# Kernel tuning notes

Measured on AMD Instinct MI355X. Metric: run time of the kernel, lower is better.

The kernel has to match this reference:

```python
import jax, jax.numpy as jnp
import numpy as np

GROUPS = 4
SF = 2   # scale_factor
K = 3    # filter_k

def conv1x1(x, w, b):
    return jnp.einsum('bchw,oc->bohw', x, w) + b[None, :, None, None]

def grid_sample(img, grid):
    # img: (N,C,H,W); grid: (N,Hg,Wg,2) xy in [-1,1]; bilinear, border padding, align_corners=False
    N, C, H, W = img.shape
    ix = jnp.clip(((grid[..., 0] + 1.0) * W - 1.0) * 0.5, 0.0, W - 1.0)
    iy = jnp.clip(((grid[..., 1] + 1.0) * H - 1.0) * 0.5, 0.0, H - 1.0)
    x0 = jnp.floor(ix); y0 = jnp.floor(iy)
    wx = (ix - x0)[..., None]; wy = (iy - y0)[..., None]
    x0i = x0.astype(jnp.int32); y0i = y0.astype(jnp.int32)
    x1i = jnp.minimum(x0i + 1, W - 1); y1i = jnp.minimum(y0i + 1, H - 1)
    bidx = jnp.arange(N)[:, None, None]
    v00 = img[bidx, :, y0i, x0i]; v01 = img[bidx, :, y0i, x1i]
    v10 = img[bidx, :, y1i, x0i]; v11 = img[bidx, :, y1i, x1i]   # (N,Hg,Wg,C)
    out = (v00 * (1 - wx) * (1 - wy) + v01 * wx * (1 - wy)
           + v10 * (1 - wx) * wy + v11 * wx * wy)
    return jnp.transpose(out, (0, 3, 1, 2))

def def_sample(x, off):
    b, c, h, w = x.shape
    g = GROUPS
    off = off.reshape(b * g, SF, SF, 2, h, w).transpose(0, 4, 1, 5, 2, 3)
    hd, wd = SF * h, SF * w
    off = off.reshape(b * g, hd, wd, 2)
    gy, gx = jnp.meshgrid(jnp.arange(hd, dtype=x.dtype) + 0.5,
                          jnp.arange(wd, dtype=x.dtype) + 0.5, indexing='ij')
    base = jnp.stack([gx, gy], axis=-1)[None]
    grid = 2.0 * (base + off) / jnp.array([wd, hd], dtype=x.dtype) - 1.0
    return grid_sample(x.reshape(b * g, c // g, h, w), grid).reshape(b, c, hd, wd)

def dyn_filter(x, compress, kw, kb):
    b, c, h, w = x.shape
    kern = jax.nn.softmax(conv1x1(compress, kw, kb), axis=1)  # (b,K*K,h,w)
    p = K // 2
    xp = jnp.pad(x, ((0, 0), (0, 0), (p, p), (p, p)))
    patches = jnp.stack([xp[:, :, dy:dy + h, dx:dx + w]
                         for dy in range(K) for dx in range(K)], axis=2)  # (b,c,K*K,h,w)
    return jnp.einsum('bkhw,bckhw->bchw', kern, patches)

def trim_op(x, toff):
    b, c, h, w = x.shape
    g = GROUPS
    off = toff.reshape(b, g, 2, h, w).transpose(0, 1, 3, 4, 2)  # (b,g,h,w,2) xy
    gy, gx = jnp.meshgrid(jnp.arange(h, dtype=x.dtype) + 0.5,
                          jnp.arange(w, dtype=x.dtype) + 0.5, indexing='ij')
    base = jnp.stack([gx, gy], axis=-1)[None, None]
    grid = (2.0 * (base + off) / jnp.array([w, h], dtype=x.dtype) - 1.0).reshape(b * g, h, w, 2)
    return grid_sample(x.reshape(b * g, c // g, h, w), grid).reshape(b, c, h, w)

def setup_inputs():
    key = jax.random.key(0)
    ks = jax.random.split(key, 13)
    C = 256
    oc = GROUPS * SF * SF * 2  # 32
    f = jnp.float32
    return {
        "x": jax.random.normal(ks[0], (4, C, 64, 64), f),
        "def_off_w": jax.random.normal(ks[1], (oc, C), f) * 0.001,
        "def_off_b": jnp.zeros((oc,), f),
        "def_ast_w": jax.random.normal(ks[2], (oc, C), f) * 0.01,
        "def_ast_b": jnp.zeros((oc,), f),
        "comp_w": jax.random.normal(ks[3], (64, C), f) * (1.0 / np.sqrt(C).astype(np.float32)),
        "comp_b": jnp.zeros((64,), f),
        "filt_w": jax.random.normal(ks[4], (K * K, 64), f) * 0.001,
        "filt_b": jnp.zeros((K * K,), f),
        "trim_w": jax.random.normal(ks[5], (GROUPS * 2, 64), f) * 0.001,
        "trim_b": jnp.zeros((GROUPS * 2,), f),
        "trim_ast_w": jax.random.normal(ks[6], (GROUPS * 2, 64), f) * 0.01,
        "trim_ast_b": jnp.zeros((GROUPS * 2,), f),
    }

def reference(x, def_off_w, def_off_b, def_ast_w, def_ast_b, comp_w, comp_b,
              filt_w, filt_b, trim_w, trim_b, trim_ast_w, trim_ast_b):
    off = conv1x1(x, def_off_w, def_off_b) * jax.nn.sigmoid(conv1x1(x, def_ast_w, def_ast_b))
    x_up = def_sample(x, off)                              # (b,c,2h,2w)
    comp = conv1x1(x_up, comp_w, comp_b)                   # (b,64,2h,2w)
    x_filt = dyn_filter(x_up, comp, filt_w, filt_b)
    toff = conv1x1(comp, trim_w, trim_b) * jax.nn.sigmoid(conv1x1(comp, trim_ast_w, trim_ast_b))
    return trim_op(x_filt, toff)
```

## Files before the change

### kernel.cpp

```cpp
#include <hip/hip_runtime.h>
#include <hip/hip_bf16.h>
#include <string.h>

typedef __hip_bfloat16 bf16;
typedef __attribute__((ext_vector_type(8))) short short8;
typedef __attribute__((ext_vector_type(4))) short short4v;
typedef __attribute__((ext_vector_type(4))) float f32x4;

__device__ __forceinline__ float s2f(short s) {
    return __uint_as_float(((unsigned)(unsigned short)s) << 16);
}
__device__ __forceinline__ short f2s(float v) {
    bf16 t = __float2bfloat16(v); short s; __builtin_memcpy(&s, &t, 2); return s;
}

#define HWD 16384

__global__ __launch_bounds__(512) void k01_xpose_off(const float* __restrict__ x,
        const float* __restrict__ w_off, const float* __restrict__ b_off,
        const float* __restrict__ w_ast, const float* __restrict__ b_ast,
        bf16* __restrict__ xpm, float* __restrict__ offpm)
{
    __shared__ __align__(16) short tileS[32 * 256];
    const int b = blockIdx.x >> 7;
    const int p0 = (blockIdx.x & 127) << 5;
    const int lane = threadIdx.x & 63;
    const int wave = threadIdx.x >> 6;
    const int n = lane & 15, quad = lane >> 4;
    const int wq = wave & 3;
    const int mh = wave >> 2;

    const int j = (wq << 4) + n, oc = j >> 1, kind = j & 1;
    short8 bfrag[8];
    const float* wrow = (kind ? w_ast : w_off) + oc * 256 + quad * 8;
#pragma unroll
    for (int kc = 0; kc < 8; ++kc) {
        float4 lo = *(const float4*)(wrow + kc * 32);
        float4 hi = *(const float4*)(wrow + kc * 32 + 4);
        short8 f;
        f[0] = f2s(lo.x); f[1] = f2s(lo.y); f[2] = f2s(lo.z); f[3] = f2s(lo.w);
        f[4] = f2s(hi.x); f[5] = f2s(hi.y); f[6] = f2s(hi.z); f[7] = f2s(hi.w);
        bfrag[kc] = f;
    }
    float bias = kind ? b_ast[oc] : b_off[oc];

    {
        const float* xb = x + ((size_t)b << 20);
        const int px = threadIdx.x & 31;
        const int gi0 = threadIdx.x >> 5;
#pragma unroll
        for (int it = 0; it < 2; ++it) {
            int gi = gi0 + (it << 4);
            int cbase = gi << 3;
            short8 pk;
#pragma unroll
            for (int jj = 0; jj < 8; ++jj)
                pk[jj] = f2s(xb[((size_t)(cbase + jj) << 12) + p0 + px]);
            int slot = gi ^ (px & 7);
            *(short8*)&tileS[(px << 8) + (slot << 3)] = pk;
        }
    }
    __syncthreads();

    {
        short* ob = (short*)xpm + ((size_t)((b << 12) + p0) << 8);
#pragma unroll
        for (int rr = 0; rr < 4; ++rr) {
            int r = (wave << 2) + rr;
            short4v v = *(const short4v*)&tileS[(r << 8)
                        + ((((lane >> 1) ^ (r & 7)) << 3) | ((lane & 1) << 2))];
            *(short4v*)(ob + ((size_t)r << 8) + (lane << 2)) = v;
        }
    }

    float* obase = offpm + ((size_t)(b << 12) << 5);
    f32x4 acc = {0.f, 0.f, 0.f, 0.f};
#pragma unroll
    for (int kc = 0; kc < 8; ++kc) {
        int slot = (((kc << 2) + quad) ^ (n & 7)) << 3;
        short8 a = *(const short8*)&tileS[((mh * 16 + n) << 8) + slot];
        acc = __builtin_amdgcn_mfma_f32_16x16x32_bf16(a, bfrag[kc], acc, 0, 0, 0);
    }
#pragma unroll
    for (int r = 0; r < 4; ++r) {
        float v0 = acc[r] + bias;
        float p0v = __shfl_xor(v0, 1, 64);
        if (!(n & 1)) {
            int px = p0 + mh * 16 + quad * 4 + r;
            obase[((size_t)px << 5) + oc] = v0 * (1.f / (1.f + expf(-p0v)));
        }
    }
}

__global__ __launch_bounds__(512, 4) void k234_defsample_comp_filter(
        const bf16* __restrict__ xpm, const float* __restrict__ offpm,
        const float* __restrict__ cw, const float* __restrict__ cb,
        const float* __restrict__ fw_g, const float* __restrict__ fb,
        const float* __restrict__ tw, const float* __restrict__ tb,
        const float* __restrict__ taw, const float* __restrict__ tab,
        bf16* __restrict__ xfilt, float* __restrict__ toff)
{
    __shared__ __align__(16) short xupS[100 * 256];
    __shared__ __align__(16) float smc[64][65];
    __shared__ __align__(16) float fwS[64 * 12];
    __shared__ __align__(16) float swS[64 * 16];
    __shared__ __align__(16) short kernS[64][24];

    for (int i = threadIdx.x; i < 64 * 12; i += 512) {
        int c = i / 12, k = i % 12;
        fwS[i] = (k < 9) ? fw_g[k * 64 + c] : 0.f;
    }
    for (int i = threadIdx.x; i < 64 * 16; i += 512) {
        int c = i >> 4, jj = i & 15;
        int oc = jj >> 1, kind = jj & 1;
        swS[i] = kind ? taw[oc * 64 + c] : tw[oc * 64 + c];
    }

    const int nb = gridDim.x >> 3;
    const int vbid = (blockIdx.x & 7) * nb + (blockIdx.x >> 3);
    const int b = vbid >> 8;
    const int tile = vbid & 255;
    const int ty = tile >> 4, tx = tile & 15;
    const int lane = threadIdx.x & 63;
    const int wave = threadIdx.x >> 6;
    const int n = lane & 15, quad = lane >> 4;
    const int wq = wave & 3, mh = wave >> 2;
    const int ocb = wq << 4;

    {
        const short* xsrc = (const short*)xpm + ((size_t)b << 20);
        const int ph = lane >> 5;
        const int cl = lane & 31;
        const int e = cl << 3;
        const int g = cl >> 3;
        const int base = (wave << 1) + ph;

        float2 fo[7];
#pragma unroll
        for (int it = 0; it < 7; ++it) {
            int l = base + (it << 4);
            if (l < 100) {
                int lhy = (l * 205) >> 11;
                int lwx = l - lhy * 10;
                int hy = min(max(ty * 8 - 1 + lhy, 0), 127);
                int wx = min(max(tx * 8 - 1 + lwx, 0), 127);
                int och = (g << 3) + ((hy & 1) << 2) + ((wx & 1) << 1);
                fo[it] = *(const float2*)(offpm
                        + ((size_t)((b << 12) + ((hy >> 1) << 6) + (wx >> 1)) << 5)
                        + och);
            }
        }

        short8 t00[4], t01[4], t10[4], t11[4];

#define K234_ISSUE(it, slot) { \
            int l = base + ((it) << 4); \
            if (l < 100) { \
                int lhy = (l * 205) >> 11; \
                int lwx = l - lhy * 10; \
                int hy = min(max(ty * 8 - 1 + lhy, 0), 127); \
                int wx = min(max(tx * 8 - 1 + lwx, 0), 127); \
                float ix = (wx + 0.5f + fo[it].x) * 0.5f - 0.5f; \
                float iy = (hy + 0.5f + fo[it].y) * 0.5f - 0.5f; \
                ix = fminf(fmaxf(ix, 0.f), 63.f); \
                iy = fminf(fmaxf(iy, 0.f), 63.f); \
                int x0 = (int)ix, y0 = (int)iy; \
                int x1 = min(x0 + 1, 63), y1 = min(y0 + 1, 63); \
                t00[slot] = *(const short8*)(xsrc + (((size_t)(y0 << 6) + x0) << 8) + e); \
                t01[slot] = *(const short8*)(xsrc + (((size_t)(y0 << 6) + x1) << 8) + e); \
                t10[slot] = *(const short8*)(xsrc + (((size_t)(y1 << 6) + x0) << 8) + e); \
                t11[slot] = *(const short8*)(xsrc + (((size_t)(y1 << 6) + x1) << 8) + e); \
            } }

#define K234_CONSUME(it, slot) { \
            int l = base + ((it) << 4); \
            if (l < 100) { \
                int lhy = (l * 205) >> 11; \
                int lwx = l - lhy * 10; \
                int hy = min(max(ty * 8 - 1 + lhy, 0), 127); \
                int wx = min(max(tx * 8 - 1 + lwx, 0), 127); \
                float ix = (wx + 0.5f + fo[it].x) * 0.5f - 0.5f; \
                float iy = (hy + 0.5f + fo[it].y) * 0.5f - 0.5f; \
                ix = fminf(fmaxf(ix, 0.f), 63.f); \
                iy = fminf(fmaxf(iy, 0.f), 63.f); \
                float fx = ix - floorf(ix), fy = iy - floorf(iy); \
                float w00 = (1.f - fx) * (1.f - fy), w01 = fx * (1.f - fy); \
                float w10 = (1.f - fx) * fy,        w11 = fx * fy; \
                short8 pk; \
                _Pragma("unroll") \
                for (int jj = 0; jj < 8; ++jj) { \
                    float v = w00 * s2f(t00[slot][jj]) + w01 * s2f(t01[slot][jj]) \
                            + w10 * s2f(t10[slot][jj]) + w11 * s2f(t11[slot][jj]); \
                    pk[jj] = f2s(v); \
                } \
                int sl2 = cl ^ (l & 7); \
                *(short8*)&xupS[(l << 8) + (sl2 << 3)] = pk; \
            } }

        K234_ISSUE(0, 0)
        K234_ISSUE(1, 1)
        K234_ISSUE(2, 2)
        K234_ISSUE(3, 3)
        K234_CONSUME(0, 0)  K234_ISSUE(4, 0)
        K234_CONSUME(1, 1)  K234_ISSUE(5, 1)
        K234_CONSUME(2, 2)  K234_ISSUE(6, 2)
        K234_CONSUME(3, 3)
        K234_CONSUME(4, 0)
        K234_CONSUME(5, 1)
        K234_CONSUME(6, 2)
#undef K234_ISSUE
#undef K234_CONSUME
    }

    short8 bfrag[8];
    {
        const float* wrow = cw + (ocb + n) * 256 + quad * 8;
#pragma unroll
        for (int kc = 0; kc < 8; ++kc) {
            float4 lo = *(const float4*)(wrow + kc * 32);
            float4 hi = *(const float4*)(wrow + kc * 32 + 4);
            short8 f;
            f[0] = f2s(lo.x); f[1] = f2s(lo.y); f[2] = f2s(lo.z); f[3] = f2s(lo.w);
            f[4] = f2s(hi.x); f[5] = f2s(hi.y); f[6] = f2s(hi.z); f[7] = f2s(hi.w);
            bfrag[kc] = f;
        }
    }
    float bias = cb[ocb + n];
    __syncthreads();

    const int m0 = mh << 5;
    const int pA = m0 + n, pB = m0 + 16 + n;
    const int rA = ((pA >> 3) + 1) * 10 + (pA & 7) + 1;
    const int rB = ((pB >> 3) + 1) * 10 + (pB & 7) + 1;
    f32x4 acc0 = {0.f,0.f,0.f,0.f}, acc1 = {0.f,0.f,0.f,0.f};
#pragma unroll
    for (int kc = 0; kc < 8; ++kc) {
        int sp = (kc << 2) + quad;
        short8 a0 = *(const short8*)&xupS[(rA << 8) + ((sp ^ (rA & 7)) << 3)];
        short8 a1 = *(const short8*)&xupS[(rB << 8) + ((sp ^ (rB & 7)) << 3)];
        acc0 = __builtin_amdgcn_mfma_f32_16x16x32_bf16(a0, bfrag[kc], acc0, 0, 0, 0);
        acc1 = __builtin_amdgcn_mfma_f32_16x16x32_bf16(a1, bfrag[kc], acc1, 0, 0, 0);
    }
#pragma unroll
    for (int r = 0; r < 4; ++r) {
        smc[m0 +      quad * 4 + r][ocb + n] = acc0[r] + bias;
        smc[m0 + 16 + quad * 4 + r][ocb + n] = acc1[r] + bias;
    }
    __syncthreads();

    const int px = lane;
    const int q = wave;
    if (q == 0) {
        float a[9];
#pragma unroll
        for (int k = 0; k < 9; ++k) a[k] = fb[k];
        for (int c = 0; c < 64; ++c) {
            float v = smc[px][c];
            const float4* wr = reinterpret_cast<const float4*>(&fwS[c * 12]);
            float4 w0 = wr[0], w1 = wr[1];
            float w8 = fwS[c * 12 + 8];
            a[0] += v * w0.x; a[1] += v * w0.y; a[2] += v * w0.z; a[3] += v * w0.w;
            a[4] += v * w1.x; a[5] += v * w1.y; a[6] += v * w1.z; a[7] += v * w1.w;
            a[8] += v * w8;
        }
        float mx = a[0];
#pragma unroll
        for (int k = 1; k < 9; ++k) mx = fmaxf(mx, a[k]);
        float s = 0.f;
#pragma unroll
        for (int k = 0; k < 9; ++k) { a[k] = expf(a[k] - mx); s += a[k]; }
        float inv = 1.f / s;
#pragma unroll
        for (int k = 0; k < 9; ++k) kernS[px][k] = f2s(a[k] * inv);
    } else if (q <= 4) {
        const int oc0 = (q - 1) << 1;
        float o[2], aa[2];
#pragma unroll
        for (int i = 0; i < 2; ++i) { o[i] = tb[oc0 + i]; aa[i] = tab[oc0 + i]; }
        for (int c = 0; c < 64; ++c) {
            float v = smc[px][c];
            const float* wr = &swS[c << 4];
#pragma unroll
            for (int i = 0; i < 2; ++i) {
                o[i]  += v * wr[2 * (oc0 + i)];
                aa[i] += v * wr[2 * (oc0 + i) + 1];
            }
        }
        int hw = ((ty * 8 + (px >> 3)) << 7) + tx * 8 + (px & 7);
#pragma unroll
        for (int i = 0; i < 2; ++i)
            toff[((size_t)((b << 3) + oc0 + i) << 14) + hw] =
                o[i] * (1.f / (1.f + expf(-aa[i])));
    }
    __syncthreads();

    {
        const int chunk = threadIdx.x & 31;
        const int pxg = threadIdx.x >> 5;
#pragma unroll
        for (int it = 0; it < 4; ++it) {
            int p = (pxg << 2) + it;
            int ly = p >> 3, lx = p & 7;
            int gh = ty * 8 + ly, gw = tx * 8 + lx;
            float wk[9];
            short8 k8 = *(const short8*)&kernS[p][0];
#pragma unroll
            for (int k = 0; k < 8; ++k) wk[k] = s2f(k8[k]);
            wk[8] = s2f(kernS[p][8]);
            float ymask[3] = { gh > 0 ? 1.f : 0.f, 1.f, gh < 127 ? 1.f : 0.f };
            float xmask[3] = { gw > 0 ? 1.f : 0.f, 1.f, gw < 127 ? 1.f : 0.f };
            float sum[8];
#pragma unroll
            for (int jj = 0; jj < 8; ++jj) sum[jj] = 0.f;
#pragma unroll
            for (int dy = 0; dy < 3; ++dy) {
#pragma unroll
                for (int dx = 0; dx < 3; ++dx) {
                    float wgt = wk[dy * 3 + dx] * ymask[dy] * xmask[dx];
                    int r = (ly + dy) * 10 + lx + dx;
                    short8 v = *(const short8*)&xupS[(r << 8)
                                + (((chunk ^ (r & 7))) << 3)];
#pragma unroll
                    for (int jj = 0; jj < 8; ++jj) sum[jj] += wgt * s2f(v[jj]);
                }
            }
            short8 pk;
#pragma unroll
            for (int jj = 0; jj < 8; ++jj) pk[jj] = f2s(sum[jj]);
            int hw = (gh << 7) + gw;
            *(short8*)((short*)xfilt + ((size_t)((b << 14) + hw) << 8)
                       + chunk * 8) = pk;
        }
    }
}

__global__ __launch_bounds__(1024, 4) void k6_trim(const bf16* __restrict__ xfilt,
        const float* __restrict__ toff, float* __restrict__ out)
{
    __shared__ __align__(16) float sm[32][258];
    const int nb = gridDim.x >> 3;
    const int vbid = (blockIdx.x & 7) * nb + (blockIdx.x >> 3);
    int b = vbid >> 9;
    int hw0 = (vbid & 511) << 5;
    int pp = threadIdx.x >> 5;
    int cl = threadIdx.x & 31;
    int e = cl << 3;
    int g = cl >> 3;
    const short* xb = (const short*)xfilt + ((size_t)(b * HWD) << 8);
    const float* tfx = toff + ((size_t)(b * 8 + 2 * g)     << 14);
    const float* tfy = toff + ((size_t)(b * 8 + 2 * g + 1) << 14);

    {
        int hw = hw0 + pp;
        int h = hw >> 7, w = hw & 127;
        float ox = tfx[hw], oy = tfy[hw];
        float ix = fminf(fmaxf(w + ox, 0.f), 127.f);
        float iy = fminf(fmaxf(h + oy, 0.f), 127.f);
        float x0f = floorf(ix), y0f = floorf(iy);
        float fx = ix - x0f, fy = iy - y0f;
        int x0 = (int)x0f, y0 = (int)y0f;
        int x1 = min(x0 + 1, 127), y1 = min(y0 + 1, 127);
        float w00 = (1.f - fx) * (1.f - fy), w01 = fx * (1.f - fy);
        float w10 = (1.f - fx) * fy,        w11 = fx * fy;
        short8 v00 = *(const short8*)(xb + (((size_t)(y0 << 7) + x0) << 8) + e);
        short8 v01 = *(const short8*)(xb + (((size_t)(y0 << 7) + x1) << 8) + e);
        short8 v10 = *(const short8*)(xb + (((size_t)(y1 << 7) + x0) << 8) + e);
        short8 v11 = *(const short8*)(xb + (((size_t)(y1 << 7) + x1) << 8) + e);
#pragma unroll
        for (int jp = 0; jp < 4; ++jp) {
            float2 t;
            t.x = w00 * s2f(v00[2*jp])   + w01 * s2f(v01[2*jp])
                + w10 * s2f(v10[2*jp])   + w11 * s2f(v11[2*jp]);
            t.y = w00 * s2f(v00[2*jp+1]) + w01 * s2f(v01[2*jp+1])
                + w10 * s2f(v10[2*jp+1]) + w11 * s2f(v11[2*jp+1]);
            *(float2*)&sm[pp][e + 2*jp] = t;
        }
    }
    __syncthreads();
    int lp = threadIdx.x & 31;
    int cg = threadIdx.x >> 5;
    float* ob = out + ((size_t)b << 22) + hw0 + lp;
#pragma unroll
    for (int k = 0; k < 8; ++k) {
        int c = (cg << 3) + k;
        ob[(size_t)c << 14] = sm[lp][c];
    }
}

extern "C" void kernel_launch(void* const* d_in, const int* in_sizes, int n_in,
                              void* d_out, int out_size, void* d_ws, size_t ws_size,
                              hipStream_t stream)
{
    const float* x       = (const float*)d_in[0];
    const float* w_off   = (const float*)d_in[1];
    const float* b_off   = (const float*)d_in[2];
    const float* w_ast   = (const float*)d_in[3];
    const float* b_ast   = (const float*)d_in[4];
    const float* comp_w  = (const float*)d_in[5];
    const float* comp_b  = (const float*)d_in[6];
    const float* filt_w  = (const float*)d_in[7];
    const float* filt_b  = (const float*)d_in[8];
    const float* trim_w  = (const float*)d_in[9];
    const float* trim_b  = (const float*)d_in[10];
    const float* trim_aw = (const float*)d_in[11];
    const float* trim_ab = (const float*)d_in[12];
    float* out = (float*)d_out;

    char* ws = (char*)d_ws;
    float* offpm = (float*)(ws);
    bf16*  xpm   = (bf16*) (ws + (2ull << 20));
    bf16*  xfilt = (bf16*) (ws + (16ull << 20));
    float* toff  = (float*)(ws + (48ull << 20));

    hipLaunchKernelGGL(k01_xpose_off, dim3(512),  dim3(512), 0, stream,
                       x, w_off, b_off, w_ast, b_ast, xpm, offpm);
    hipLaunchKernelGGL(k234_defsample_comp_filter, dim3(1024), dim3(512), 0, stream,
                       xpm, offpm, comp_w, comp_b, filt_w, filt_b,
                       trim_w, trim_b, trim_aw, trim_ab, xfilt, toff);
    hipLaunchKernelGGL(k6_trim,     dim3(2048),  dim3(1024), 0, stream,
                       xfilt, toff, out);
}
```

Measured before the change: 167.2 us.

## Halve fused defsample/comp/filter tile to 8x4 pixels for higher occupancy

The fused deformable-sample, compress-conv and dynamic-filter kernel now processes 4x8 output tiles instead of 8x8. Shared memory drops (xupS from 100 to 60 halo rows), the grid doubles to 2048 blocks and launch bounds ask for 6 blocks per CU. The MFMA, softmax and trim-offset phases are rebalanced to 32 pixels per block. In exchange the halo overhead per output pixel rises (60/32 vs 100/64), so more gather loads happen, and each wave does less work per phase, with fewer loads in flight per wave.

```diff
diff --git a/kernel.cpp b/kernel.cpp
--- a/kernel.cpp
+++ b/kernel.cpp
@@ -92,7 +92,7 @@
     }
 }
 
-__global__ __launch_bounds__(512, 4) void k234_defsample_comp_filter(
+__global__ __launch_bounds__(512, 6) void k234_defsample_comp_filter(
         const bf16* __restrict__ xpm, const float* __restrict__ offpm,
         const float* __restrict__ cw, const float* __restrict__ cb,
         const float* __restrict__ fw_g, const float* __restrict__ fb,
@@ -100,11 +100,11 @@
         const float* __restrict__ taw, const float* __restrict__ tab,
         bf16* __restrict__ xfilt, float* __restrict__ toff)
 {
-    __shared__ __align__(16) short xupS[100 * 256];
-    __shared__ __align__(16) float smc[64][65];
+    __shared__ __align__(16) short xupS[60 * 256];
+    __shared__ __align__(16) float smc[32][65];
     __shared__ __align__(16) float fwS[64 * 12];
     __shared__ __align__(16) float swS[64 * 16];
-    __shared__ __align__(16) short kernS[64][24];
+    __shared__ __align__(16) short kernS[32][24];
 
     for (int i = threadIdx.x; i < 64 * 12; i += 512) {
         int c = i / 12, k = i % 12;
@@ -118,8 +118,8 @@
 
     const int nb = gridDim.x >> 3;
     const int vbid = (blockIdx.x & 7) * nb + (blockIdx.x >> 3);
-    const int b = vbid >> 8;
-    const int tile = vbid & 255;
+    const int b = vbid >> 9;
+    const int tile = vbid & 511;
     const int ty = tile >> 4, tx = tile & 15;
     const int lane = threadIdx.x & 63;
     const int wave = threadIdx.x >> 6;
@@ -135,14 +135,14 @@
         const int g = cl >> 3;
         const int base = (wave << 1) + ph;
 
-        float2 fo[7];
-#pragma unroll
-        for (int it = 0; it < 7; ++it) {
+        float2 fo[4];
+#pragma unroll
+        for (int it = 0; it < 4; ++it) {
             int l = base + (it << 4);
-            if (l < 100) {
+            if (l < 60) {
                 int lhy = (l * 205) >> 11;
                 int lwx = l - lhy * 10;
-                int hy = min(max(ty * 8 - 1 + lhy, 0), 127);
+                int hy = min(max(ty * 4 - 1 + lhy, 0), 127);
                 int wx = min(max(tx * 8 - 1 + lwx, 0), 127);
                 int och = (g << 3) + ((hy & 1) << 2) + ((wx & 1) << 1);
                 fo[it] = *(const float2*)(offpm
@@ -151,14 +151,14 @@
             }
         }
 
-        short8 t00[4], t01[4], t10[4], t11[4];
+        short8 t00[2], t01[2], t10[2], t11[2];
 
 #define K234_ISSUE(it, slot) { \
             int l = base + ((it) << 4); \
-            if (l < 100) { \
+            if (l < 60) { \
                 int lhy = (l * 205) >> 11; \
                 int lwx = l - lhy * 10; \
-                int hy = min(max(ty * 8 - 1 + lhy, 0), 127); \
+                int hy = min(max(ty * 4 - 1 + lhy, 0), 127); \
                 int wx = min(max(tx * 8 - 1 + lwx, 0), 127); \
                 float ix = (wx + 0.5f + fo[it].x) * 0.5f - 0.5f; \
                 float iy = (hy + 0.5f + fo[it].y) * 0.5f - 0.5f; \
@@ -174,10 +174,10 @@
 
 #define K234_CONSUME(it, slot) { \
             int l = base + ((it) << 4); \
-            if (l < 100) { \
+            if (l < 60) { \
                 int lhy = (l * 205) >> 11; \
                 int lwx = l - lhy * 10; \
-                int hy = min(max(ty * 8 - 1 + lhy, 0), 127); \
+                int hy = min(max(ty * 4 - 1 + lhy, 0), 127); \
                 int wx = min(max(tx * 8 - 1 + lwx, 0), 127); \
                 float ix = (wx + 0.5f + fo[it].x) * 0.5f - 0.5f; \
                 float iy = (hy + 0.5f + fo[it].y) * 0.5f - 0.5f; \
@@ -199,15 +199,10 @@
 
         K234_ISSUE(0, 0)
         K234_ISSUE(1, 1)
-        K234_ISSUE(2, 2)
-        K234_ISSUE(3, 3)
-        K234_CONSUME(0, 0)  K234_ISSUE(4, 0)
-        K234_CONSUME(1, 1)  K234_ISSUE(5, 1)
-        K234_CONSUME(2, 2)  K234_ISSUE(6, 2)
-        K234_CONSUME(3, 3)
-        K234_CONSUME(4, 0)
-        K234_CONSUME(5, 1)
-        K234_CONSUME(6, 2)
+        K234_CONSUME(0, 0)  K234_ISSUE(2, 0)
+        K234_CONSUME(1, 1)  K234_ISSUE(3, 1)
+        K234_CONSUME(2, 0)
+        K234_CONSUME(3, 1)
 #undef K234_ISSUE
 #undef K234_CONSUME
     }
@@ -228,69 +223,59 @@
     float bias = cb[ocb + n];
     __syncthreads();
 
-    const int m0 = mh << 5;
-    const int pA = m0 + n, pB = m0 + 16 + n;
+    const int m0 = mh << 4;
+    const int pA = m0 + n;
     const int rA = ((pA >> 3) + 1) * 10 + (pA & 7) + 1;
-    const int rB = ((pB >> 3) + 1) * 10 + (pB & 7) + 1;
-    f32x4 acc0 = {0.f,0.f,0.f,0.f}, acc1 = {0.f,0.f,0.f,0.f};
+    f32x4 acc = {0.f,0.f,0.f,0.f};
 #pragma unroll
     for (int kc = 0; kc < 8; ++kc) {
         int sp = (kc << 2) + quad;
-        short8 a0 = *(const short8*)&xupS[(rA << 8) + ((sp ^ (rA & 7)) << 3)];
-        short8 a1 = *(const short8*)&xupS[(rB << 8) + ((sp ^ (rB & 7)) << 3)];
-        acc0 = __builtin_amdgcn_mfma_f32_16x16x32_bf16(a0, bfrag[kc], acc0, 0, 0, 0);
-        acc1 = __builtin_amdgcn_mfma_f32_16x16x32_bf16(a1, bfrag[kc], acc1, 0, 0, 0);
-    }
-#pragma unroll
-    for (int r = 0; r < 4; ++r) {
-        smc[m0 +      quad * 4 + r][ocb + n] = acc0[r] + bias;
-        smc[m0 + 16 + quad * 4 + r][ocb + n] = acc1[r] + bias;
-    }
+        short8 a = *(const short8*)&xupS[(rA << 8) + ((sp ^ (rA & 7)) << 3)];
+        acc = __builtin_amdgcn_mfma_f32_16x16x32_bf16(a, bfrag[kc], acc, 0, 0, 0);
+    }
+#pragma unroll
+    for (int r = 0; r < 4; ++r)
+        smc[m0 + quad * 4 + r][ocb + n] = acc[r] + bias;
     __syncthreads();
 
-    const int px = lane;
     const int q = wave;
     if (q == 0) {
-        float a[9];
-#pragma unroll
-        for (int k = 0; k < 9; ++k) a[k] = fb[k];
+        if (lane < 32) {
+            const int px = lane;
+            float a[9];
+#pragma unroll
+            for (int k = 0; k < 9; ++k) a[k] = fb[k];
+            for (int c = 0; c < 64; ++c) {
+                float v = smc[px][c];
+                const float4* wr = reinterpret_cast<const float4*>(&fwS[c * 12]);
+                float4 w0 = wr[0], w1 = wr[1];
+                float w8 = fwS[c * 12 + 8];
+                a[0] += v * w0.x; a[1] += v * w0.y; a[2] += v * w0.z; a[3] += v * w0.w;
+                a[4] += v * w1.x; a[5] += v * w1.y; a[6] += v * w1.z; a[7] += v * w1.w;
+                a[8] += v * w8;
+            }
+            float mx = a[0];
+#pragma unroll
+            for (int k = 1; k < 9; ++k) mx = fmaxf(mx, a[k]);
+            float s = 0.f;
+#pragma unroll
+            for (int k = 0; k < 9; ++k) { a[k] = expf(a[k] - mx); s += a[k]; }
+            float inv = 1.f / s;
+#pragma unroll
+            for (int k = 0; k < 9; ++k) kernS[px][k] = f2s(a[k] * inv);
+        }
+    } else if (q <= 4) {
+        const int px = lane & 31;
+        const int oc = ((q - 1) << 1) | (lane >> 5);
+        float o = tb[oc], aa = tab[oc];
         for (int c = 0; c < 64; ++c) {
             float v = smc[px][c];
-            const float4* wr = reinterpret_cast<const float4*>(&fwS[c * 12]);
-            float4 w0 = wr[0], w1 = wr[1];
-            float w8 = fwS[c * 12 + 8];
-            a[0] += v * w0.x; a[1] += v * w0.y; a[2] += v * w0.z; a[3] += v * w0.w;
-            a[4] += v * w1.x; a[5] += v * w1.y; a[6] += v * w1.z; a[7] += v * w1.w;
-            a[8] += v * w8;
-        }
-        float mx = a[0];
-#pragma unroll
-        for (int k = 1; k < 9; ++k) mx = fmaxf(mx, a[k]);
-        float s = 0.f;
-#pragma unroll
-        for (int k = 0; k < 9; ++k) { a[k] = expf(a[k] - mx); s += a[k]; }
-        float inv = 1.f / s;
-#pragma unroll
-        for (int k = 0; k < 9; ++k) kernS[px][k] = f2s(a[k] * inv);
-    } else if (q <= 4) {
-        const int oc0 = (q - 1) << 1;
-        float o[2], aa[2];
-#pragma unroll
-        for (int i = 0; i < 2; ++i) { o[i] = tb[oc0 + i]; aa[i] = tab[oc0 + i]; }
-        for (int c = 0; c < 64; ++c) {
-            float v = smc[px][c];
-            const float* wr = &swS[c << 4];
-#pragma unroll
-            for (int i = 0; i < 2; ++i) {
-                o[i]  += v * wr[2 * (oc0 + i)];
-                aa[i] += v * wr[2 * (oc0 + i) + 1];
-            }
-        }
-        int hw = ((ty * 8 + (px >> 3)) << 7) + tx * 8 + (px & 7);
-#pragma unroll
-        for (int i = 0; i < 2; ++i)
-            toff[((size_t)((b << 3) + oc0 + i) << 14) + hw] =
-                o[i] * (1.f / (1.f + expf(-aa[i])));
+            o  += v * swS[(c << 4) + 2 * oc];
+            aa += v * swS[(c << 4) + 2 * oc + 1];
+        }
+        int hw = ((ty * 4 + (px >> 3)) << 7) + tx * 8 + (px & 7);
+        toff[((size_t)((b << 3) + oc) << 14) + hw] =
+            o * (1.f / (1.f + expf(-aa)));
     }
     __syncthreads();
 
@@ -298,10 +283,10 @@
         const int chunk = threadIdx.x & 31;
         const int pxg = threadIdx.x >> 5;
 #pragma unroll
-        for (int it = 0; it < 4; ++it) {
-            int p = (pxg << 2) + it;
+        for (int it = 0; it < 2; ++it) {
+            int p = (pxg << 1) + it;
             int ly = p >> 3, lx = p & 7;
-            int gh = ty * 8 + ly, gw = tx * 8 + lx;
+            int gh = ty * 4 + ly, gw = tx * 8 + lx;
             float wk[9];
             short8 k8 = *(const short8*)&kernS[p][0];
 #pragma unroll
@@ -414,7 +399,7 @@
 
     hipLaunchKernelGGL(k01_xpose_off, dim3(512),  dim3(512), 0, stream,
                        x, w_off, b_off, w_ast, b_ast, xpm, offpm);
-    hipLaunchKernelGGL(k234_defsample_comp_filter, dim3(1024), dim3(512), 0, stream,
+    hipLaunchKernelGGL(k234_defsample_comp_filter, dim3(2048), dim3(512), 0, stream,
                        xpm, offpm, comp_w, comp_b, filt_w, filt_b,
                        trim_w, trim_b, trim_aw, trim_ab, xfilt, toff);
     hipLaunchKernelGGL(k6_trim,     dim3(2048),  dim3(1024), 0, stream,
```

Result: slower. 183.2 us (+9.6%).
